# Optimization experiments

Measured on AMD Instinct MI355X. Metric: run time of the kernel, lower is better.

The kernel has to match this reference:

```python
import jax, jax.numpy as jnp
import numpy as np

T, B = 4096, 8192


def setup_inputs() -> dict:
    key = jax.random.key(0)
    k1, k2 = jax.random.split(key)
    # binary Bernoulli(0.5) observations, shape [T, B, 1]
    inputs = jnp.round(jax.random.uniform(k1, (T, B, 1), dtype=jnp.float32))
    # decay_rate = exp(-1 / 10**loglifetime), loglifetime ~ U(0.5, 2.5)
    loglifetime = jax.random.uniform(k2, (), minval=0.5, maxval=2.5)
    decay_rate = jnp.exp(-1.0 / (10.0 ** loglifetime)).astype(jnp.float32)
    return {"inputs": inputs, "decay_rate": decay_rate}


def _forward(inputs, decay_rate):
    # order == 1 ('transition' estimate): bigram leaky counts
    x = inputs[:, :, 0]                      # [T, B]
    n_seqs = x.shape[1]
    z = jnp.zeros((n_seqs,), dtype=inputs.dtype)
    d = decay_rate

    def step(carry, x_t):
        n10, n11, na0, na1, prev = carry
        n10 = d * (n10 + x_t * (1.0 - prev))   # ones after a 0
        n11 = d * (n11 + x_t * prev)           # ones after a 1
        na0 = d * (na0 + (1.0 - prev))         # all after a 0
        na1 = d * (na1 + prev)                 # all after a 1
        return (n10, n11, na0, na1, x_t), (n10, n11, na0, na1)

    _, (n10s, n11s, na0s, na1s) = jax.lax.scan(step, (z, z, z, z, z), x)

    N_ONES_PRIOR, N_ALL_PRIOR = 1.0, 2.0
    p0 = (n10s + N_ONES_PRIOR) / (na0s + N_ALL_PRIOR)   # [T, B]
    p1 = (n11s + N_ONES_PRIOR) / (na1s + N_ALL_PRIOR)   # [T, B]
    # prediction conditioned on current observation
    pred = p0 * (1.0 - x) + p1 * x                      # [T, B]
    return pred[:, :, None]                             # [T, B, 1]


def reference(inputs, decay_rate):
    return _forward(inputs, decay_rate)
```

## Files before the change

kernel.cpp:

```cpp
#include <hip/hip_runtime.h>


constexpr int T_DIM  = 4096;
constexpr int B_DIM  = 8192;
constexpr int NCHUNK = 64;
constexpr int CLEN   = T_DIM / NCHUNK;
constexpr int VEC    = 4;


__global__ __launch_bounds__(256) void partial_kernel(
    const float* __restrict__ x, const float* __restrict__ dptr,
    float* __restrict__ ws)
{
    const float d  = *dptr;
    const int   c  = blockIdx.y;
    const int   b0 = (blockIdx.x * blockDim.x + threadIdx.x) * VEC;
    const long  t0 = (long)c * CLEN;

    float prev[VEC];
    if (c == 0) {
        prev[0] = prev[1] = prev[2] = prev[3] = 0.0f;
    } else {
        const float4 pv = *reinterpret_cast<const float4*>(x + (t0 - 1) * B_DIM + b0);
        prev[0] = pv.x; prev[1] = pv.y; prev[2] = pv.z; prev[3] = pv.w;
    }

    float n10[VEC] = {0,0,0,0}, n11[VEC] = {0,0,0,0};
    float na0[VEC] = {0,0,0,0}, na1[VEC] = {0,0,0,0};

    const float* p = x + t0 * B_DIM + b0;
    for (int k = 0; k < CLEN; ++k) {
        const float4 xv = *reinterpret_cast<const float4*>(p);
        p += B_DIM;
        const float xs[VEC] = {xv.x, xv.y, xv.z, xv.w};
        #pragma unroll
        for (int j = 0; j < VEC; ++j) {
            const float xt = xs[j];
            const float pr = prev[j];
            const float om = 1.0f - pr;
            n10[j] = d * (n10[j] + xt * om);
            n11[j] = d * (n11[j] + xt * pr);
            na0[j] = d * (na0[j] + om);
            na1[j] = d * (na1[j] + pr);
            prev[j] = xt;
        }
    }

    float* w = ws + (size_t)c * B_DIM + b0;
    *reinterpret_cast<float4*>(w + (size_t)0 * NCHUNK * B_DIM) = make_float4(n10[0], n10[1], n10[2], n10[3]);
    *reinterpret_cast<float4*>(w + (size_t)1 * NCHUNK * B_DIM) = make_float4(n11[0], n11[1], n11[2], n11[3]);
    *reinterpret_cast<float4*>(w + (size_t)2 * NCHUNK * B_DIM) = make_float4(na0[0], na0[1], na0[2], na0[3]);
    *reinterpret_cast<float4*>(w + (size_t)3 * NCHUNK * B_DIM) = make_float4(na1[0], na1[1], na1[2], na1[3]);
}

__global__ __launch_bounds__(256) void scan_kernel(
    const float* __restrict__ dptr, float* __restrict__ ws)
{
    const float d  = *dptr;
    const float dL = __powf(d, (float)CLEN);
    const int   b  = blockIdx.x * blockDim.x + threadIdx.x;
    if (b >= B_DIM) return;

    float s0 = 0.f, s1 = 0.f, s2 = 0.f, s3 = 0.f;
    for (int c = 0; c < NCHUNK; ++c) {
        float* p0 = ws + ((size_t)0 * NCHUNK + c) * B_DIM + b;
        float* p1 = ws + ((size_t)1 * NCHUNK + c) * B_DIM + b;
        float* p2 = ws + ((size_t)2 * NCHUNK + c) * B_DIM + b;
        float* p3 = ws + ((size_t)3 * NCHUNK + c) * B_DIM + b;
        const float l0 = *p0, l1 = *p1, l2 = *p2, l3 = *p3;
        *p0 = s0; *p1 = s1; *p2 = s2; *p3 = s3;
        s0 = dL * s0 + l0;
        s1 = dL * s1 + l1;
        s2 = dL * s2 + l2;
        s3 = dL * s3 + l3;
    }
}

__global__ __launch_bounds__(256) void final_kernel(
    const float* __restrict__ x, const float* __restrict__ dptr,
    const float* __restrict__ ws, float* __restrict__ out)
{
    const float d  = *dptr;
    const int   c  = blockIdx.y;
    const int   b0 = (blockIdx.x * blockDim.x + threadIdx.x) * VEC;
    const long  t0 = (long)c * CLEN;

    float prev[VEC];
    if (c == 0) {
        prev[0] = prev[1] = prev[2] = prev[3] = 0.0f;
    } else {
        const float4 pv = *reinterpret_cast<const float4*>(x + (t0 - 1) * B_DIM + b0);
        prev[0] = pv.x; prev[1] = pv.y; prev[2] = pv.z; prev[3] = pv.w;
    }

    const float* w = ws + (size_t)c * B_DIM + b0;
    const float4 s0 = *reinterpret_cast<const float4*>(w + (size_t)0 * NCHUNK * B_DIM);
    const float4 s1 = *reinterpret_cast<const float4*>(w + (size_t)1 * NCHUNK * B_DIM);
    const float4 s2 = *reinterpret_cast<const float4*>(w + (size_t)2 * NCHUNK * B_DIM);
    const float4 s3 = *reinterpret_cast<const float4*>(w + (size_t)3 * NCHUNK * B_DIM);
    float n10[VEC] = {s0.x, s0.y, s0.z, s0.w};
    float n11[VEC] = {s1.x, s1.y, s1.z, s1.w};
    float na0[VEC] = {s2.x, s2.y, s2.z, s2.w};
    float na1[VEC] = {s3.x, s3.y, s3.z, s3.w};

    const float* p = x + t0 * B_DIM + b0;
    float*       q = out + t0 * B_DIM + b0;
    for (int k = 0; k < CLEN; ++k) {
        const float4 xv = *reinterpret_cast<const float4*>(p);
        p += B_DIM;
        const float xs[VEC] = {xv.x, xv.y, xv.z, xv.w};
        float pr4[VEC];
        #pragma unroll
        for (int j = 0; j < VEC; ++j) {
            const float xt = xs[j];
            const float pv = prev[j];
            const float om = 1.0f - pv;
            n10[j] = d * (n10[j] + xt * om);
            n11[j] = d * (n11[j] + xt * pv);
            na0[j] = d * (na0[j] + om);
            na1[j] = d * (na1[j] + pv);
            prev[j] = xt;
            const float p0 = (n10[j] + 1.0f) * __builtin_amdgcn_rcpf(na0[j] + 2.0f);
            const float p1 = (n11[j] + 1.0f) * __builtin_amdgcn_rcpf(na1[j] + 2.0f);
            pr4[j] = p0 + (p1 - p0) * xt;
        }
        *reinterpret_cast<float4*>(q) = make_float4(pr4[0], pr4[1], pr4[2], pr4[3]);
        q += B_DIM;
    }
}

extern "C" void kernel_launch(void* const* d_in, const int* in_sizes, int n_in,
                              void* d_out, int out_size, void* d_ws, size_t ws_size,
                              hipStream_t stream) {
    const float* x  = (const float*)d_in[0];
    const float* dr = (const float*)d_in[1];
    float* ws  = (float*)d_ws;
    float* out = (float*)d_out;

    dim3 blk(256);
    dim3 grid1(B_DIM / VEC / 256, NCHUNK);
    partial_kernel<<<grid1, blk, 0, stream>>>(x, dr, ws);
    scan_kernel<<<B_DIM / 256, blk, 0, stream>>>(dr, ws);
    final_kernel<<<grid1, blk, 0, stream>>>(x, dr, ws, out);
}
```

Before: 279.3 us.

## Narrow per-thread width, batch loads ahead, parallelize scan across counters

Each thread now handles 2 sequences instead of 4, which doubles the thread count in the partial and final kernels. Eight timesteps of input are loaded up front before the recurrence runs, so more loads are in flight. The scan kernel gives each of the four counters its own thread, which quadruples its parallelism, and computes d^64 by repeated squaring. In exchange, float2 accesses are narrower than float4 and each thread holds more registers for the batched loads.

```diff
diff --git a/kernel.cpp b/kernel.cpp
--- a/kernel.cpp
+++ b/kernel.cpp
@@ -5,7 +5,8 @@
 constexpr int B_DIM  = 8192;
 constexpr int NCHUNK = 64;
 constexpr int CLEN   = T_DIM / NCHUNK;
-constexpr int VEC    = 4;
+constexpr int VEC    = 2;
+constexpr int UNROLL = 8;
 
 
 __global__ __launch_bounds__(256) void partial_kernel(
@@ -19,60 +20,60 @@
 
     float prev[VEC];
     if (c == 0) {
-        prev[0] = prev[1] = prev[2] = prev[3] = 0.0f;
+        prev[0] = prev[1] = 0.0f;
     } else {
-        const float4 pv = *reinterpret_cast<const float4*>(x + (t0 - 1) * B_DIM + b0);
-        prev[0] = pv.x; prev[1] = pv.y; prev[2] = pv.z; prev[3] = pv.w;
+        const float2 pv = *reinterpret_cast<const float2*>(x + (t0 - 1) * B_DIM + b0);
+        prev[0] = pv.x; prev[1] = pv.y;
     }
 
-    float n10[VEC] = {0,0,0,0}, n11[VEC] = {0,0,0,0};
-    float na0[VEC] = {0,0,0,0}, na1[VEC] = {0,0,0,0};
+    float n10[VEC] = {0,0}, n11[VEC] = {0,0}, na0[VEC] = {0,0}, na1[VEC] = {0,0};
 
     const float* p = x + t0 * B_DIM + b0;
-    for (int k = 0; k < CLEN; ++k) {
-        const float4 xv = *reinterpret_cast<const float4*>(p);
-        p += B_DIM;
-        const float xs[VEC] = {xv.x, xv.y, xv.z, xv.w};
+    for (int kk = 0; kk < CLEN; kk += UNROLL) {
+        float2 xv[UNROLL];
         #pragma unroll
-        for (int j = 0; j < VEC; ++j) {
-            const float xt = xs[j];
-            const float pr = prev[j];
-            const float om = 1.0f - pr;
-            n10[j] = d * (n10[j] + xt * om);
-            n11[j] = d * (n11[j] + xt * pr);
-            na0[j] = d * (na0[j] + om);
-            na1[j] = d * (na1[j] + pr);
-            prev[j] = xt;
+        for (int u = 0; u < UNROLL; ++u)
+            xv[u] = *reinterpret_cast<const float2*>(p + (size_t)u * B_DIM);
+        p += (size_t)UNROLL * B_DIM;
+        #pragma unroll
+        for (int u = 0; u < UNROLL; ++u) {
+            const float xs[VEC] = {xv[u].x, xv[u].y};
+            #pragma unroll
+            for (int j = 0; j < VEC; ++j) {
+                const float xt = xs[j];
+                const float pr = prev[j];
+                const float om = 1.0f - pr;
+                n10[j] = d * (n10[j] + xt * om);
+                n11[j] = d * (n11[j] + xt * pr);
+                na0[j] = d * (na0[j] + om);
+                na1[j] = d * (na1[j] + pr);
+                prev[j] = xt;
+            }
         }
     }
 
     float* w = ws + (size_t)c * B_DIM + b0;
-    *reinterpret_cast<float4*>(w + (size_t)0 * NCHUNK * B_DIM) = make_float4(n10[0], n10[1], n10[2], n10[3]);
-    *reinterpret_cast<float4*>(w + (size_t)1 * NCHUNK * B_DIM) = make_float4(n11[0], n11[1], n11[2], n11[3]);
-    *reinterpret_cast<float4*>(w + (size_t)2 * NCHUNK * B_DIM) = make_float4(na0[0], na0[1], na0[2], na0[3]);
-    *reinterpret_cast<float4*>(w + (size_t)3 * NCHUNK * B_DIM) = make_float4(na1[0], na1[1], na1[2], na1[3]);
+    *reinterpret_cast<float2*>(w + (size_t)0 * NCHUNK * B_DIM) = make_float2(n10[0], n10[1]);
+    *reinterpret_cast<float2*>(w + (size_t)1 * NCHUNK * B_DIM) = make_float2(n11[0], n11[1]);
+    *reinterpret_cast<float2*>(w + (size_t)2 * NCHUNK * B_DIM) = make_float2(na0[0], na0[1]);
+    *reinterpret_cast<float2*>(w + (size_t)3 * NCHUNK * B_DIM) = make_float2(na1[0], na1[1]);
 }
 
 __global__ __launch_bounds__(256) void scan_kernel(
     const float* __restrict__ dptr, float* __restrict__ ws)
 {
-    const float d  = *dptr;
-    const float dL = __powf(d, (float)CLEN);
-    const int   b  = blockIdx.x * blockDim.x + threadIdx.x;
-    if (b >= B_DIM) return;
+    float dL = *dptr;
+    #pragma unroll
+    for (int i = 0; i < 6; ++i) dL = dL * dL;
 
-    float s0 = 0.f, s1 = 0.f, s2 = 0.f, s3 = 0.f;
+    const int tid = blockIdx.x * blockDim.x + threadIdx.x;
+    float* p = ws + (size_t)(tid / B_DIM) * NCHUNK * B_DIM + (tid % B_DIM);
+
+    float s = 0.f;
     for (int c = 0; c < NCHUNK; ++c) {
-        float* p0 = ws + ((size_t)0 * NCHUNK + c) * B_DIM + b;
-        float* p1 = ws + ((size_t)1 * NCHUNK + c) * B_DIM + b;
-        float* p2 = ws + ((size_t)2 * NCHUNK + c) * B_DIM + b;
-        float* p3 = ws + ((size_t)3 * NCHUNK + c) * B_DIM + b;
-        const float l0 = *p0, l1 = *p1, l2 = *p2, l3 = *p3;
-        *p0 = s0; *p1 = s1; *p2 = s2; *p3 = s3;
-        s0 = dL * s0 + l0;
-        s1 = dL * s1 + l1;
-        s2 = dL * s2 + l2;
-        s3 = dL * s3 + l3;
+        const float l = p[(size_t)c * B_DIM];
+        p[(size_t)c * B_DIM] = s;
+        s = dL * s + l;
     }
 }
 
@@ -87,45 +88,51 @@
 
     float prev[VEC];
     if (c == 0) {
-        prev[0] = prev[1] = prev[2] = prev[3] = 0.0f;
+        prev[0] = prev[1] = 0.0f;
     } else {
-        const float4 pv = *reinterpret_cast<const float4*>(x + (t0 - 1) * B_DIM + b0);
-        prev[0] = pv.x; prev[1] = pv.y; prev[2] = pv.z; prev[3] = pv.w;
+        const float2 pv = *reinterpret_cast<const float2*>(x + (t0 - 1) * B_DIM + b0);
+        prev[0] = pv.x; prev[1] = pv.y;
     }
 
     const float* w = ws + (size_t)c * B_DIM + b0;
-    const float4 s0 = *reinterpret_cast<const float4*>(w + (size_t)0 * NCHUNK * B_DIM);
-    const float4 s1 = *reinterpret_cast<const float4*>(w + (size_t)1 * NCHUNK * B_DIM);
-    const float4 s2 = *reinterpret_cast<const float4*>(w + (size_t)2 * NCHUNK * B_DIM);
-    const float4 s3 = *reinterpret_cast<const float4*>(w + (size_t)3 * NCHUNK * B_DIM);
-    float n10[VEC] = {s0.x, s0.y, s0.z, s0.w};
-    float n11[VEC] = {s1.x, s1.y, s1.z, s1.w};
-    float na0[VEC] = {s2.x, s2.y, s2.z, s2.w};
-    float na1[VEC] = {s3.x, s3.y, s3.z, s3.w};
+    const float2 s0 = *reinterpret_cast<const float2*>(w + (size_t)0 * NCHUNK * B_DIM);
+    const float2 s1 = *reinterpret_cast<const float2*>(w + (size_t)1 * NCHUNK * B_DIM);
+    const float2 s2 = *reinterpret_cast<const float2*>(w + (size_t)2 * NCHUNK * B_DIM);
+    const float2 s3 = *reinterpret_cast<const float2*>(w + (size_t)3 * NCHUNK * B_DIM);
+    float n10[VEC] = {s0.x, s0.y};
+    float n11[VEC] = {s1.x, s1.y};
+    float na0[VEC] = {s2.x, s2.y};
+    float na1[VEC] = {s3.x, s3.y};
 
-    const float* p = x + t0 * B_DIM + b0;
+    const float* p = x   + t0 * B_DIM + b0;
     float*       q = out + t0 * B_DIM + b0;
-    for (int k = 0; k < CLEN; ++k) {
-        const float4 xv = *reinterpret_cast<const float4*>(p);
-        p += B_DIM;
-        const float xs[VEC] = {xv.x, xv.y, xv.z, xv.w};
-        float pr4[VEC];
+    for (int kk = 0; kk < CLEN; kk += UNROLL) {
+        float2 xv[UNROLL];
         #pragma unroll
-        for (int j = 0; j < VEC; ++j) {
-            const float xt = xs[j];
-            const float pv = prev[j];
-            const float om = 1.0f - pv;
-            n10[j] = d * (n10[j] + xt * om);
-            n11[j] = d * (n11[j] + xt * pv);
-            na0[j] = d * (na0[j] + om);
-            na1[j] = d * (na1[j] + pv);
-            prev[j] = xt;
-            const float p0 = (n10[j] + 1.0f) * __builtin_amdgcn_rcpf(na0[j] + 2.0f);
-            const float p1 = (n11[j] + 1.0f) * __builtin_amdgcn_rcpf(na1[j] + 2.0f);
-            pr4[j] = p0 + (p1 - p0) * xt;
+        for (int u = 0; u < UNROLL; ++u)
+            xv[u] = *reinterpret_cast<const float2*>(p + (size_t)u * B_DIM);
+        p += (size_t)UNROLL * B_DIM;
+        #pragma unroll
+        for (int u = 0; u < UNROLL; ++u) {
+            const float xs[VEC] = {xv[u].x, xv[u].y};
+            float pr2[VEC];
+            #pragma unroll
+            for (int j = 0; j < VEC; ++j) {
+                const float xt = xs[j];
+                const float pv = prev[j];
+                const float om = 1.0f - pv;
+                n10[j] = d * (n10[j] + xt * om);
+                n11[j] = d * (n11[j] + xt * pv);
+                na0[j] = d * (na0[j] + om);
+                na1[j] = d * (na1[j] + pv);
+                prev[j] = xt;
+                const float p0 = (n10[j] + 1.0f) * __builtin_amdgcn_rcpf(na0[j] + 2.0f);
+                const float p1 = (n11[j] + 1.0f) * __builtin_amdgcn_rcpf(na1[j] + 2.0f);
+                pr2[j] = p0 + (p1 - p0) * xt;
+            }
+            *reinterpret_cast<float2*>(q + (size_t)u * B_DIM) = make_float2(pr2[0], pr2[1]);
         }
-        *reinterpret_cast<float4*>(q) = make_float4(pr4[0], pr4[1], pr4[2], pr4[3]);
-        q += B_DIM;
+        q += (size_t)UNROLL * B_DIM;
     }
 }
 
@@ -140,6 +147,6 @@
     dim3 blk(256);
     dim3 grid1(B_DIM / VEC / 256, NCHUNK);
     partial_kernel<<<grid1, blk, 0, stream>>>(x, dr, ws);
-    scan_kernel<<<B_DIM / 256, blk, 0, stream>>>(dr, ws);
+    scan_kernel<<<(4 * B_DIM) / 256, blk, 0, stream>>>(dr, ws);
     final_kernel<<<grid1, blk, 0, stream>>>(x, dr, ws, out);
 }
```

New measurement: 264.7 us. -5.2%, faster.
